# Optimization experiments

Hardware: AMD Instinct MI355X
Metric: run time of the kernel (lower is better)

Reference implementation:

```python
import jax, jax.numpy as jnp
import numpy as np

N_QUBITS = 10
DIM = 2 ** N_QUBITS
W_MUL = (2.0 ** 0.5) * (5.0 ** -0.5)  # he_std with gain=sqrt(2), use_wscale=True, lrmul=1
_X = jnp.array([[0.0, 1.0], [1.0, 0.0]], dtype=jnp.complex64)
_XX = jnp.kron(_X, _X)  # 4x4
_I4 = jnp.eye(4, dtype=jnp.complex64)


def _ry(theta):
    c = jnp.cos(theta / 2)
    s = jnp.sin(theta / 2)
    return jnp.stack([jnp.stack([c, -s]), jnp.stack([s, c])]).astype(jnp.complex64)


def _rxx(theta):
    c = jnp.cos(theta / 2).astype(jnp.complex64)
    s = jnp.sin(theta / 2).astype(jnp.complex64)
    return c * _I4 - 1j * s * _XX


def _apply_1q(M, g, q):
    # left-multiply kron-expanded 1-qubit gate on qubit q (qubit 0 = most significant)
    Mr = M.reshape((2,) * N_QUBITS + (DIM,))
    Mr = jnp.tensordot(g, Mr, axes=((1,), (q,)))
    Mr = jnp.moveaxis(Mr, 0, q)
    return Mr.reshape(DIM, DIM)


def _apply_2q(M, g4, q1, q2):
    g = g4.reshape(2, 2, 2, 2)
    Mr = M.reshape((2,) * N_QUBITS + (DIM,))
    Mr = jnp.tensordot(g, Mr, axes=((2, 3), (q1, q2)))
    Mr = jnp.moveaxis(Mr, (0, 1), (q1, q2))
    return Mr.reshape(DIM, DIM)


def _circuit_unitary(weight):
    w = weight * W_MUL
    U = jnp.eye(DIM, dtype=jnp.complex64)
    for q in range(0, N_QUBITS, 2):
        U = _apply_1q(U, _ry(w[0]), q)
        U = _apply_1q(U, _ry(w[1]), q + 1)
        U = _apply_2q(U, _rxx(w[2]), q, q + 1)
        U = _apply_1q(U, _ry(w[3]), q)
        U = _apply_1q(U, _ry(w[4]), q + 1)
        U = _apply_2q(U, _rxx(w[5]), q, q + 1)
    return U


def setup_inputs() -> dict:
    key = jax.random.key(0)
    k1, k2 = jax.random.split(key)
    x = jax.random.normal(k1, (8, DIM, DIM), dtype=jnp.float32)
    weight = jax.random.uniform(k2, (6,), dtype=jnp.float32, minval=0.0, maxval=2.0 * np.pi)
    return {"x": x, "weight": weight}


def reference(x, weight):
    U = _circuit_unitary(weight)
    xc = x.astype(jnp.complex64)
    # forward: dag(U) @ x @ U  (broadcast over batch)
    out = jnp.matmul(jnp.matmul(U.conj().T, xc), U)
    # return real/imag stacked so output is real-dtype
    return jnp.stack([out.real, out.imag])
```

## Files before the change

kernel.cpp:

```cpp
#include <hip/hip_runtime.h>
#include <hip/hip_fp16.h>

#define DIM 1024
#define NB 8
#define CBLK 8
#define LSTRIDE 9

typedef float vfloat4 __attribute__((ext_vector_type(4)));

__device__ __forceinline__ int lidx(int r, int c) {
  return r * LSTRIDE + c;
}

__device__ __forceinline__ unsigned rflu(unsigned x) {
  return (unsigned)__builtin_amdgcn_readfirstlane((int)x);
}
__device__ __forceinline__ unsigned h2u(__half2 h) {
  union { __half2 h; unsigned u; } c; c.h = h; return c.u;
}
__device__ __forceinline__ __half2 u2h(unsigned u) {
  union { unsigned u; __half2 h; } c; c.u = u; return c.h;
}
__device__ __forceinline__ __half2 h2swap(__half2 x) {
  unsigned u = h2u(x);
  return u2h((u >> 16) | (u << 16));
}

struct __align__(16) H2x4 { __half2 h[4]; };

__device__ __forceinline__ void mv4p(__half2* v, const int stride,
                                     const unsigned (&Wre2)[4][4],
                                     const unsigned (&Wimn)[4][4]) {
  __half2 x0 = v[0], x1 = v[stride], x2 = v[2 * stride], x3 = v[3 * stride];
  __half2 s0 = h2swap(x0), s1 = h2swap(x1), s2 = h2swap(x2), s3 = h2swap(x3);
  #pragma unroll
  for (int p = 0; p < 4; ++p) {
    __half2 a = u2h(Wre2[p][0]) * x0;
    a = __hfma2(u2h(Wimn[p][0]), s0, a);
    a = __hfma2(u2h(Wre2[p][2]), x2, a);
    a = __hfma2(u2h(Wimn[p][2]), s2, a);
    __half2 b = u2h(Wre2[p][1]) * x1;
    b = __hfma2(u2h(Wimn[p][1]), s1, b);
    b = __hfma2(u2h(Wre2[p][3]), x3, b);
    b = __hfma2(u2h(Wimn[p][3]), s3, b);
    v[p * stride] = a + b;
  }
}

__device__ __forceinline__ void mv4rp(const __half2* x, __half2* y,
                                      const unsigned (&Wri)[4][4]) {
  #pragma unroll
  for (int p = 0; p < 4; ++p) {
    __half2 a = u2h(Wri[p][0]) * x[0];
    a = __hfma2(u2h(Wri[p][2]), x[2], a);
    __half2 b = u2h(Wri[p][1]) * x[1];
    b = __hfma2(u2h(Wri[p][3]), x[3], b);
    y[p] = a + b;
  }
}

__device__ void compute_W(const float* __restrict__ wgt, int pass,
                          unsigned (&Wre2)[4][4], unsigned (&Wimn)[4][4],
                          unsigned (&Wri)[4][4]) {
  const float WMUL = 0.6324555320336759f;
  float ca[6], sa[6];
  #pragma unroll
  for (int i = 0; i < 6; ++i) {
    float h = wgt[i] * (0.5f * WMUL);
    ca[i] = cosf(h);
    sa[i] = sinf(h);
  }
  float R01[4][4], R34[4][4];
  {
    float a0[2][2] = {{ca[0], -sa[0]}, {sa[0], ca[0]}};
    float b0[2][2] = {{ca[1], -sa[1]}, {sa[1], ca[1]}};
    float a1[2][2] = {{ca[3], -sa[3]}, {sa[3], ca[3]}};
    float b1[2][2] = {{ca[4], -sa[4]}, {sa[4], ca[4]}};
    #pragma unroll
    for (int i = 0; i < 4; ++i)
      #pragma unroll
      for (int j = 0; j < 4; ++j) {
        R01[i][j] = a0[i >> 1][j >> 1] * b0[i & 1][j & 1];
        R34[i][j] = a1[i >> 1][j >> 1] * b1[i & 1][j & 1];
      }
  }
  float M2re[4][4], M2im[4][4];
  #pragma unroll
  for (int k = 0; k < 4; ++k)
    #pragma unroll
    for (int j = 0; j < 4; ++j) {
      M2re[k][j] = ca[2] * R01[k][j];
      M2im[k][j] = -sa[2] * R01[3 - k][j];
    }
  float M3re[4][4], M3im[4][4];
  #pragma unroll
  for (int i = 0; i < 4; ++i)
    #pragma unroll
    for (int j = 0; j < 4; ++j) {
      float rr = 0.f, ii = 0.f;
      #pragma unroll
      for (int k = 0; k < 4; ++k) {
        rr += R34[i][k] * M2re[k][j];
        ii += R34[i][k] * M2im[k][j];
      }
      M3re[i][j] = rr;
      M3im[i][j] = ii;
    }
  #pragma unroll
  for (int k = 0; k < 4; ++k)
    #pragma unroll
    for (int j = 0; j < 4; ++j) {
      float vre = ca[5] * M3re[k][j] + sa[5] * M3im[3 - k][j];
      float vim = ca[5] * M3im[k][j] - sa[5] * M3re[3 - k][j];
      float wim = (pass == 0) ? -vim : vim;
      Wre2[j][k] = rflu(h2u(__floats2half2_rn(vre, vre)));
      Wimn[j][k] = rflu(h2u(__floats2half2_rn(-wim, wim)));
      Wri[j][k] = rflu(h2u(__floats2half2_rn(vre, wim)));
    }
}

template <int PASS>
__global__ __launch_bounds__(512, 4) void qpass(const void* __restrict__ srcv,
                                                const float* __restrict__ weight,
                                                void* __restrict__ dstv,
                                                int batch0) {
  __shared__ __half2 tile[DIM * LSTRIDE];
  const int t = threadIdx.x;

  int B = blockIdx.x;
  int total = gridDim.x;
  int L;
  if ((total & 7) == 0) {
    int q = total >> 3;
    L = (B & 7) * q + (B >> 3);
  } else {
    L = B;
  }
  const int cg = L & 127;
  const int bl = L >> 7;
  const int bg = batch0 + bl;
  const int c0 = cg * CBLK;

  unsigned Wre2[4][4], Wimn[4][4], Wri[4][4];
  compute_W(weight, PASS, Wre2, Wimn, Wri);

  if (PASS == 0) {
    const float* s = (const float*)srcv + (size_t)bg * DIM * DIM + c0;
    #pragma unroll
    for (int it = 0; it < 4; ++it) {
      int u = it * 512 + t;
      int r = u >> 1, h = (u & 1) * 4;
      float4 v = *reinterpret_cast<const float4*>(s + (size_t)r * DIM + h);
      tile[lidx(r, h + 0)] = __half2half2(__float2half(v.x));
      tile[lidx(r, h + 1)] = __half2half2(__float2half(v.y));
      tile[lidx(r, h + 2)] = __half2half2(__float2half(v.z));
      tile[lidx(r, h + 3)] = __half2half2(__float2half(v.w));
    }
  } else {
    const __half2* s = (const __half2*)srcv + ((size_t)bl << 20) + c0;
    #pragma unroll
    for (int it = 0; it < 4; ++it) {
      int u = it * 512 + t;
      int r = u >> 1, h = (u & 1) * 4;
      H2x4 v = *reinterpret_cast<const H2x4*>(s + (size_t)r * DIM + h);
      tile[lidx(r, h + 0)] = v.h[0];
      tile[lidx(r, h + 1)] = v.h[1];
      tile[lidx(r, h + 2)] = v.h[2];
      tile[lidx(r, h + 3)] = v.h[3];
    }
  }
  __syncthreads();

  {
    int c = t & 7, g = t >> 3;
    __half2 v[16];
    if (PASS == 0) {
      #pragma unroll
      for (int k0 = 0; k0 < 4; ++k0) {
        __half2 xs[4];
        #pragma unroll
        for (int k1 = 0; k1 < 4; ++k1)
          xs[k1] = tile[lidx(g + k0 * 256 + k1 * 64, c)];
        mv4rp(xs, &v[k0 * 4], Wri);
      }
    } else {
      #pragma unroll
      for (int k0 = 0; k0 < 4; ++k0)
        #pragma unroll
        for (int k1 = 0; k1 < 4; ++k1)
          v[k0 * 4 + k1] = tile[lidx(g + k0 * 256 + k1 * 64, c)];
      #pragma unroll
      for (int k0 = 0; k0 < 4; ++k0) mv4p(&v[k0 * 4], 1, Wre2, Wimn);
    }
    #pragma unroll
    for (int k1 = 0; k1 < 4; ++k1) mv4p(&v[k1], 4, Wre2, Wimn);
    #pragma unroll
    for (int k0 = 0; k0 < 4; ++k0)
      #pragma unroll
      for (int k1 = 0; k1 < 4; ++k1)
        tile[lidx(g + k0 * 256 + k1 * 64, c)] = v[k0 * 4 + k1];
  }
  __syncthreads();

  {
    int c = t & 7, g = t >> 3;
    int base = (g >> 2) * 64 + (g & 3);
    __half2 v[16];
    #pragma unroll
    for (int k2 = 0; k2 < 4; ++k2)
      #pragma unroll
      for (int k3 = 0; k3 < 4; ++k3)
        v[k2 * 4 + k3] = tile[lidx(base + k2 * 16 + k3 * 4, c)];
    #pragma unroll
    for (int k2 = 0; k2 < 4; ++k2) mv4p(&v[k2 * 4], 1, Wre2, Wimn);
    #pragma unroll
    for (int k3 = 0; k3 < 4; ++k3) mv4p(&v[k3], 4, Wre2, Wimn);
    #pragma unroll
    for (int k2 = 0; k2 < 4; ++k2)
      #pragma unroll
      for (int k3 = 0; k3 < 4; ++k3)
        tile[lidx(base + k2 * 16 + k3 * 4, c)] = v[k2 * 4 + k3];
  }
  __syncthreads();

  #pragma unroll
  for (int it = 0; it < 4; ++it) {
    int c = t & 7;
    int g = (t >> 3) + 64 * it;
    __half2 v[4];
    #pragma unroll
    for (int k = 0; k < 4; ++k) v[k] = tile[lidx(4 * g + k, c)];
    mv4p(v, 1, Wre2, Wimn);
    if (PASS == 0) {
      __half2* d = (__half2*)dstv + ((size_t)bl << 20) + (size_t)(c0 + c) * DIM + 4 * g;
      H2x4 o;
      o.h[0] = v[0]; o.h[1] = v[1]; o.h[2] = v[2]; o.h[3] = v[3];
      *reinterpret_cast<H2x4*>(d) = o;
    } else {
      float2 f0 = __half22float2(v[0]), f1 = __half22float2(v[1]);
      float2 f2 = __half22float2(v[2]), f3 = __half22float2(v[3]);
      float* dr = (float*)dstv + ((size_t)bg << 20) + (size_t)(c0 + c) * DIM + 4 * g;
      float* di = dr + ((size_t)1 << 23);
      vfloat4 re = {f0.x, f1.x, f2.x, f3.x};
      vfloat4 im = {f0.y, f1.y, f2.y, f3.y};
      __builtin_nontemporal_store(re, reinterpret_cast<vfloat4*>(dr));
      __builtin_nontemporal_store(im, reinterpret_cast<vfloat4*>(di));
    }
  }
}

extern "C" void kernel_launch(void* const* d_in, const int* in_sizes, int n_in,
                              void* d_out, int out_size, void* d_ws, size_t ws_size,
                              hipStream_t stream) {
  const float* x = (const float*)d_in[0];
  const float* w = (const float*)d_in[1];

  const size_t per_batch = (size_t)DIM * DIM * sizeof(__half2);
  int max_nb = (int)(ws_size / per_batch);
  if (max_nb > NB) max_nb = NB;
  if (max_nb < 1) max_nb = 1;

  for (int b0 = 0; b0 < NB; b0 += max_nb) {
    int nb = NB - b0 < max_nb ? NB - b0 : max_nb;
    dim3 grid(128 * nb);
    qpass<0><<<grid, 512, 0, stream>>>(x, w, d_ws, b0);
    qpass<1><<<grid, 512, 0, stream>>>(d_ws, w, d_out, b0);
  }
}
```

Baseline: 53.41 us.

## Process two column tiles per block with staggered double-buffered LDS stages

Each block now handles 16 columns as two 8-column tiles in separate LDS buffers, halving the grid. The stages are skewed so that stage1 of tile A overlaps the global loads of tile B, and the write-out of tile A overlaps compute on tile B. This aims to hide global memory latency and amortize the per-block weight computation. It doubles LDS per block to about 72KB, which may reduce occupancy, and halves the number of blocks.

New measurement: 54.65 us. 1.02x slower.

```diff
diff --git a/kernel.cpp b/kernel.cpp
--- a/kernel.cpp
+++ b/kernel.cpp
@@ -5,6 +5,8 @@
 #define NB 8
 #define CBLK 8
 #define LSTRIDE 9
+#define TILE_ELEMS (DIM * LSTRIDE)
+#define LDS_BYTES (2 * TILE_ELEMS * 4)
 
 typedef float vfloat4 __attribute__((ext_vector_type(4)));
 
@@ -119,12 +121,103 @@
     }
 }
 
+
+template <int PASS>
+__device__ __forceinline__ void stage1(__half2* __restrict__ tile, int t,
+                                       const unsigned (&Wre2)[4][4],
+                                       const unsigned (&Wimn)[4][4],
+                                       const unsigned (&Wri)[4][4]) {
+  int c = t & 7, g = t >> 3;
+  __half2 v[16];
+  if (PASS == 0) {
+    #pragma unroll
+    for (int k0 = 0; k0 < 4; ++k0) {
+      __half2 xs[4];
+      #pragma unroll
+      for (int k1 = 0; k1 < 4; ++k1)
+        xs[k1] = tile[lidx(g + k0 * 256 + k1 * 64, c)];
+      mv4rp(xs, &v[k0 * 4], Wri);
+    }
+  } else {
+    #pragma unroll
+    for (int k0 = 0; k0 < 4; ++k0)
+      #pragma unroll
+      for (int k1 = 0; k1 < 4; ++k1)
+        v[k0 * 4 + k1] = tile[lidx(g + k0 * 256 + k1 * 64, c)];
+    #pragma unroll
+    for (int k0 = 0; k0 < 4; ++k0) mv4p(&v[k0 * 4], 1, Wre2, Wimn);
+  }
+  #pragma unroll
+  for (int k1 = 0; k1 < 4; ++k1) mv4p(&v[k1], 4, Wre2, Wimn);
+  #pragma unroll
+  for (int k0 = 0; k0 < 4; ++k0)
+    #pragma unroll
+    for (int k1 = 0; k1 < 4; ++k1)
+      tile[lidx(g + k0 * 256 + k1 * 64, c)] = v[k0 * 4 + k1];
+}
+
+__device__ __forceinline__ void stage2(__half2* __restrict__ tile, int t,
+                                       const unsigned (&Wre2)[4][4],
+                                       const unsigned (&Wimn)[4][4]) {
+  int c = t & 7, g = t >> 3;
+  int base = (g >> 2) * 64 + (g & 3);
+  __half2 v[16];
+  #pragma unroll
+  for (int k2 = 0; k2 < 4; ++k2)
+    #pragma unroll
+    for (int k3 = 0; k3 < 4; ++k3)
+      v[k2 * 4 + k3] = tile[lidx(base + k2 * 16 + k3 * 4, c)];
+  #pragma unroll
+  for (int k2 = 0; k2 < 4; ++k2) mv4p(&v[k2 * 4], 1, Wre2, Wimn);
+  #pragma unroll
+  for (int k3 = 0; k3 < 4; ++k3) mv4p(&v[k3], 4, Wre2, Wimn);
+  #pragma unroll
+  for (int k2 = 0; k2 < 4; ++k2)
+    #pragma unroll
+    for (int k3 = 0; k3 < 4; ++k3)
+      tile[lidx(base + k2 * 16 + k3 * 4, c)] = v[k2 * 4 + k3];
+}
+
+template <int PASS>
+__device__ __forceinline__ void stage3w(__half2* __restrict__ tile, int t,
+                                        int cb, int bl, int bg,
+                                        void* __restrict__ dstv,
+                                        const unsigned (&Wre2)[4][4],
+                                        const unsigned (&Wimn)[4][4]) {
+  #pragma unroll
+  for (int it = 0; it < 4; ++it) {
+    int c = t & 7;
+    int g = (t >> 3) + 64 * it;
+    __half2 v[4];
+    #pragma unroll
+    for (int k = 0; k < 4; ++k) v[k] = tile[lidx(4 * g + k, c)];
+    mv4p(v, 1, Wre2, Wimn);
+    if (PASS == 0) {
+      __half2* d = (__half2*)dstv + ((size_t)bl << 20) + (size_t)(cb + c) * DIM + 4 * g;
+      H2x4 o;
+      o.h[0] = v[0]; o.h[1] = v[1]; o.h[2] = v[2]; o.h[3] = v[3];
+      *reinterpret_cast<H2x4*>(d) = o;
+    } else {
+      float2 f0 = __half22float2(v[0]), f1 = __half22float2(v[1]);
+      float2 f2 = __half22float2(v[2]), f3 = __half22float2(v[3]);
+      float* dr = (float*)dstv + ((size_t)bg << 20) + (size_t)(cb + c) * DIM + 4 * g;
+      float* di = dr + ((size_t)1 << 23);
+      vfloat4 re = {f0.x, f1.x, f2.x, f3.x};
+      vfloat4 im = {f0.y, f1.y, f2.y, f3.y};
+      __builtin_nontemporal_store(re, reinterpret_cast<vfloat4*>(dr));
+      __builtin_nontemporal_store(im, reinterpret_cast<vfloat4*>(di));
+    }
+  }
+}
+
 template <int PASS>
 __global__ __launch_bounds__(512, 4) void qpass(const void* __restrict__ srcv,
                                                 const float* __restrict__ weight,
                                                 void* __restrict__ dstv,
                                                 int batch0) {
-  __shared__ __half2 tile[DIM * LSTRIDE];
+  extern __shared__ __half2 lds[];
+  __half2* tileA = lds;
+  __half2* tileB = lds + TILE_ELEMS;
   const int t = threadIdx.x;
 
   int B = blockIdx.x;
@@ -136,117 +229,91 @@
   } else {
     L = B;
   }
-  const int cg = L & 127;
-  const int bl = L >> 7;
+  const int m = L & 63;
+  const int bl = L >> 6;
   const int bg = batch0 + bl;
-  const int c0 = cg * CBLK;
+  const int c0 = m * 16;
 
   unsigned Wre2[4][4], Wimn[4][4], Wri[4][4];
   compute_W(weight, PASS, Wre2, Wimn, Wri);
 
+  const int r0 = t >> 1;
+  const int h = (t & 1) * 4;
+
   if (PASS == 0) {
-    const float* s = (const float*)srcv + (size_t)bg * DIM * DIM + c0;
-    #pragma unroll
-    for (int it = 0; it < 4; ++it) {
-      int u = it * 512 + t;
-      int r = u >> 1, h = (u & 1) * 4;
-      float4 v = *reinterpret_cast<const float4*>(s + (size_t)r * DIM + h);
-      tile[lidx(r, h + 0)] = __half2half2(__float2half(v.x));
-      tile[lidx(r, h + 1)] = __half2half2(__float2half(v.y));
-      tile[lidx(r, h + 2)] = __half2half2(__float2half(v.z));
-      tile[lidx(r, h + 3)] = __half2half2(__float2half(v.w));
+    const float* sp0 = (const float*)srcv + (size_t)bg * DIM * DIM +
+                       (size_t)r0 * DIM + h;
+    {
+      const float* sp = sp0 + c0;
+      float4 l0 = *reinterpret_cast<const float4*>(sp);
+      float4 l1 = *reinterpret_cast<const float4*>(sp + (size_t)256 * DIM);
+      float4 l2 = *reinterpret_cast<const float4*>(sp + (size_t)512 * DIM);
+      float4 l3 = *reinterpret_cast<const float4*>(sp + (size_t)768 * DIM);
+#define COMMIT0(TILE, L, RK)                                              \
+      {                                                                   \
+        (TILE)[lidx((RK), h + 0)] = __half2half2(__float2half((L).x));    \
+        (TILE)[lidx((RK), h + 1)] = __half2half2(__float2half((L).y));    \
+        (TILE)[lidx((RK), h + 2)] = __half2half2(__float2half((L).z));    \
+        (TILE)[lidx((RK), h + 3)] = __half2half2(__float2half((L).w));    \
+      }
+      COMMIT0(tileA, l0, r0) COMMIT0(tileA, l1, r0 + 256)
+      COMMIT0(tileA, l2, r0 + 512) COMMIT0(tileA, l3, r0 + 768)
+    }
+    __syncthreads();
+    {
+      const float* sp = sp0 + c0 + 8;
+      float4 l0 = *reinterpret_cast<const float4*>(sp);
+      float4 l1 = *reinterpret_cast<const float4*>(sp + (size_t)256 * DIM);
+      float4 l2 = *reinterpret_cast<const float4*>(sp + (size_t)512 * DIM);
+      float4 l3 = *reinterpret_cast<const float4*>(sp + (size_t)768 * DIM);
+      stage1<0>(tileA, t, Wre2, Wimn, Wri);
+      COMMIT0(tileB, l0, r0) COMMIT0(tileB, l1, r0 + 256)
+      COMMIT0(tileB, l2, r0 + 512) COMMIT0(tileB, l3, r0 + 768)
+#undef COMMIT0
     }
   } else {
-    const __half2* s = (const __half2*)srcv + ((size_t)bl << 20) + c0;
-    #pragma unroll
-    for (int it = 0; it < 4; ++it) {
-      int u = it * 512 + t;
-      int r = u >> 1, h = (u & 1) * 4;
-      H2x4 v = *reinterpret_cast<const H2x4*>(s + (size_t)r * DIM + h);
-      tile[lidx(r, h + 0)] = v.h[0];
-      tile[lidx(r, h + 1)] = v.h[1];
-      tile[lidx(r, h + 2)] = v.h[2];
-      tile[lidx(r, h + 3)] = v.h[3];
+    const __half2* sp0 = (const __half2*)srcv + ((size_t)bl << 20) +
+                         (size_t)r0 * DIM + h;
+    {
+      const __half2* sp = sp0 + c0;
+      H2x4 l0 = *reinterpret_cast<const H2x4*>(sp);
+      H2x4 l1 = *reinterpret_cast<const H2x4*>(sp + (size_t)256 * DIM);
+      H2x4 l2 = *reinterpret_cast<const H2x4*>(sp + (size_t)512 * DIM);
+      H2x4 l3 = *reinterpret_cast<const H2x4*>(sp + (size_t)768 * DIM);
+#define COMMIT1(TILE, L, RK)                                              \
+      {                                                                   \
+        (TILE)[lidx((RK), h + 0)] = (L).h[0];                             \
+        (TILE)[lidx((RK), h + 1)] = (L).h[1];                             \
+        (TILE)[lidx((RK), h + 2)] = (L).h[2];                             \
+        (TILE)[lidx((RK), h + 3)] = (L).h[3];                             \
+      }
+      COMMIT1(tileA, l0, r0) COMMIT1(tileA, l1, r0 + 256)
+      COMMIT1(tileA, l2, r0 + 512) COMMIT1(tileA, l3, r0 + 768)
+    }
+    __syncthreads();
+    {
+      const __half2* sp = sp0 + c0 + 8;
+      H2x4 l0 = *reinterpret_cast<const H2x4*>(sp);
+      H2x4 l1 = *reinterpret_cast<const H2x4*>(sp + (size_t)256 * DIM);
+      H2x4 l2 = *reinterpret_cast<const H2x4*>(sp + (size_t)512 * DIM);
+      H2x4 l3 = *reinterpret_cast<const H2x4*>(sp + (size_t)768 * DIM);
+      stage1<1>(tileA, t, Wre2, Wimn, Wri);
+      COMMIT1(tileB, l0, r0) COMMIT1(tileB, l1, r0 + 256)
+      COMMIT1(tileB, l2, r0 + 512) COMMIT1(tileB, l3, r0 + 768)
+#undef COMMIT1
     }
   }
   __syncthreads();
 
-  {
-    int c = t & 7, g = t >> 3;
-    __half2 v[16];
-    if (PASS == 0) {
-      #pragma unroll
-      for (int k0 = 0; k0 < 4; ++k0) {
-        __half2 xs[4];
-        #pragma unroll
-        for (int k1 = 0; k1 < 4; ++k1)
-          xs[k1] = tile[lidx(g + k0 * 256 + k1 * 64, c)];
-        mv4rp(xs, &v[k0 * 4], Wri);
-      }
-    } else {
-      #pragma unroll
-      for (int k0 = 0; k0 < 4; ++k0)
-        #pragma unroll
-        for (int k1 = 0; k1 < 4; ++k1)
-          v[k0 * 4 + k1] = tile[lidx(g + k0 * 256 + k1 * 64, c)];
-      #pragma unroll
-      for (int k0 = 0; k0 < 4; ++k0) mv4p(&v[k0 * 4], 1, Wre2, Wimn);
-    }
-    #pragma unroll
-    for (int k1 = 0; k1 < 4; ++k1) mv4p(&v[k1], 4, Wre2, Wimn);
-    #pragma unroll
-    for (int k0 = 0; k0 < 4; ++k0)
-      #pragma unroll
-      for (int k1 = 0; k1 < 4; ++k1)
-        tile[lidx(g + k0 * 256 + k1 * 64, c)] = v[k0 * 4 + k1];
-  }
+  stage1<PASS>(tileB, t, Wre2, Wimn, Wri);
+  stage2(tileA, t, Wre2, Wimn);
   __syncthreads();
 
-  {
-    int c = t & 7, g = t >> 3;
-    int base = (g >> 2) * 64 + (g & 3);
-    __half2 v[16];
-    #pragma unroll
-    for (int k2 = 0; k2 < 4; ++k2)
-      #pragma unroll
-      for (int k3 = 0; k3 < 4; ++k3)
-        v[k2 * 4 + k3] = tile[lidx(base + k2 * 16 + k3 * 4, c)];
-    #pragma unroll
-    for (int k2 = 0; k2 < 4; ++k2) mv4p(&v[k2 * 4], 1, Wre2, Wimn);
-    #pragma unroll
-    for (int k3 = 0; k3 < 4; ++k3) mv4p(&v[k3], 4, Wre2, Wimn);
-    #pragma unroll
-    for (int k2 = 0; k2 < 4; ++k2)
-      #pragma unroll
-      for (int k3 = 0; k3 < 4; ++k3)
-        tile[lidx(base + k2 * 16 + k3 * 4, c)] = v[k2 * 4 + k3];
-  }
+  stage2(tileB, t, Wre2, Wimn);
+  stage3w<PASS>(tileA, t, c0, bl, bg, dstv, Wre2, Wimn);
   __syncthreads();
 
-  #pragma unroll
-  for (int it = 0; it < 4; ++it) {
-    int c = t & 7;
-    int g = (t >> 3) + 64 * it;
-    __half2 v[4];
-    #pragma unroll
-    for (int k = 0; k < 4; ++k) v[k] = tile[lidx(4 * g + k, c)];
-    mv4p(v, 1, Wre2, Wimn);
-    if (PASS == 0) {
-      __half2* d = (__half2*)dstv + ((size_t)bl << 20) + (size_t)(c0 + c) * DIM + 4 * g;
-      H2x4 o;
-      o.h[0] = v[0]; o.h[1] = v[1]; o.h[2] = v[2]; o.h[3] = v[3];
-      *reinterpret_cast<H2x4*>(d) = o;
-    } else {
-      float2 f0 = __half22float2(v[0]), f1 = __half22float2(v[1]);
-      float2 f2 = __half22float2(v[2]), f3 = __half22float2(v[3]);
-      float* dr = (float*)dstv + ((size_t)bg << 20) + (size_t)(c0 + c) * DIM + 4 * g;
-      float* di = dr + ((size_t)1 << 23);
-      vfloat4 re = {f0.x, f1.x, f2.x, f3.x};
-      vfloat4 im = {f0.y, f1.y, f2.y, f3.y};
-      __builtin_nontemporal_store(re, reinterpret_cast<vfloat4*>(dr));
-      __builtin_nontemporal_store(im, reinterpret_cast<vfloat4*>(di));
-    }
-  }
+  stage3w<PASS>(tileB, t, c0 + 8, bl, bg, dstv, Wre2, Wimn);
 }
 
 extern "C" void kernel_launch(void* const* d_in, const int* in_sizes, int n_in,
@@ -262,8 +329,8 @@
 
   for (int b0 = 0; b0 < NB; b0 += max_nb) {
     int nb = NB - b0 < max_nb ? NB - b0 : max_nb;
-    dim3 grid(128 * nb);
-    qpass<0><<<grid, 512, 0, stream>>>(x, w, d_ws, b0);
-    qpass<1><<<grid, 512, 0, stream>>>(d_ws, w, d_out, b0);
-  }
-}
+    dim3 grid(64 * nb);
+    qpass<0><<<grid, 512, LDS_BYTES, stream>>>(x, w, d_ws, b0);
+    qpass<1><<<grid, 512, LDS_BYTES, stream>>>(d_ws, w, d_out, b0);
+  }
+}
```
